# Kernel tuning notes

Measured on AMD Instinct MI355X. Metric: run time of the kernel, lower is better.

## Reference

```python
import jax, jax.numpy as jnp
import numpy as np

B = 128
NHEAD = 16
D_MODEL = 512
D_IN = 256  # each of f_* and f_*_out; concat -> 512
N_ATOM = 128


def _scopes():
    lens = np.array([96 + (i % 33) for i in range(B)], dtype=np.int64)  # max == 128 == N_ATOM
    starts_a = np.concatenate([[1], 1 + np.cumsum(lens)[:-1]]).astype(np.int64)
    nb = 2 * lens
    starts_b = np.concatenate([[1], 1 + np.cumsum(nb)[:-1]]).astype(np.int64)
    return lens, starts_a, nb, starts_b


def setup_inputs() -> dict:
    key = jax.random.key(0)
    ks = jax.random.split(key, 10)
    lens, starts_a, nb, starts_b = _scopes()
    Na = int(1 + lens.sum())   # 14279 (row 0 is padding)
    Nb = int(1 + nb.sum())     # 28557 (bond 0 is padding)
    f_atoms = jax.random.normal(ks[0], (Na, D_IN), jnp.float32)
    f_bonds = jax.random.normal(ks[1], (Nb, D_IN), jnp.float32)
    f_atoms_out = jax.random.normal(ks[2], (Na, D_IN), jnp.float32)
    f_bonds_out = jax.random.normal(ks[3], (Nb, D_IN), jnp.float32)
    b2a = jax.random.randint(ks[4], (Nb,), 0, 96, jnp.int64 if jax.config.jax_enable_x64 else jnp.int32)
    b2revb = jax.random.randint(ks[5], (Nb,), 0, Nb, b2a.dtype)
    a_scope = jnp.stack([jnp.asarray(starts_a), jnp.asarray(lens)], axis=1)
    b_scope = jnp.stack([jnp.asarray(starts_b), jnp.asarray(nb)], axis=1)
    W_atom = jax.random.normal(ks[6], (2 * D_IN, D_MODEL), jnp.float32) * 0.02
    b_atom = jnp.zeros((D_MODEL,), jnp.float32)
    W_bond = jax.random.normal(ks[7], (2 * D_IN, NHEAD), jnp.float32) * 0.02
    b_bond = jnp.zeros((NHEAD,), jnp.float32)
    return {"f_atoms": f_atoms, "f_bonds": f_bonds, "f_atoms_out": f_atoms_out,
            "f_bonds_out": f_bonds_out, "b2a": b2a, "b2revb": b2revb,
            "a_scope": a_scope, "b_scope": b_scope, "n_atom": N_ATOM,
            "W_atom": W_atom, "b_atom": b_atom, "W_bond": W_bond, "b_bond": b_bond}


def reference(f_atoms, f_bonds, f_atoms_out, f_bonds_out, b2a, b2revb,
              a_scope, b_scope, n_atom, W_atom, b_atom, W_bond, b_bond):
    Bsz = a_scope.shape[0]
    # atom embedding: concat + linear, drop padding row 0, pad per-molecule -> [n_atom, B, d]
    atoms = jnp.concatenate([f_atoms, f_atoms_out], axis=1) @ W_atom + b_atom  # [Na, d]
    starts_a, lens_a = a_scope[:, 0], a_scope[:, 1]
    pos = jnp.arange(n_atom)
    valid = pos[None, :] < lens_a[:, None]                       # [B, n_atom]
    gidx = jnp.where(valid, starts_a[:, None] + pos[None, :], 0)  # safe gather idx
    atoms_pad = jnp.where(valid[..., None], atoms[gidx], 0.0)     # [B, n_atom, d]
    atoms_emb = atoms_pad.transpose(1, 0, 2)                      # [n_atom, B, d] (batch_first=False)
    # bond embedding -> scatter into dense pairwise matrix
    bonds = jnp.concatenate([f_bonds, f_bonds_out], axis=1) @ W_bond + b_bond  # [Nb, nhead]
    Nb = bonds.shape[0]
    starts_b = b_scope[:, 0]
    mol = jnp.searchsorted(starts_b, jnp.arange(Nb), side='right') - 1  # molecule id per bond (-1 for pad bond 0)
    offset = jnp.maximum(mol, 0) * (n_atom * n_atom)
    idx = b2a + b2a[b2revb] * n_atom + offset                     # flat index into [B*n_atom*n_atom]
    flat = jnp.zeros((Bsz * n_atom * n_atom, bonds.shape[1]), bonds.dtype).at[idx].set(bonds)
    apairs = flat.reshape(Bsz, n_atom, n_atom, -1)                # [B, n_atom, n_atom, nhead]
    padding_mask = ~valid                                         # [B, n_atom], True = pad
    apairs = jnp.where(padding_mask[:, None, :, None], -jnp.inf, apairs)
    apairs = apairs.transpose(0, 3, 1, 2)                         # [B, nhead, n_atom, n_atom]
    return atoms_emb, apairs, padding_mask
```

## Files before the change

kernel.cpp:

```cpp
#include <hip/hip_runtime.h>
#include <math.h>

#define NEG_BIG (-1e30f)

typedef __attribute__((ext_vector_type(8))) short short8;
typedef __attribute__((ext_vector_type(4))) float floatx4;

__device__ __forceinline__ unsigned short f2bf(float x) {
    unsigned u = __float_as_uint(x);
    unsigned r = (u + 0x7fffu + ((u >> 16) & 1u)) >> 16;
    return (unsigned short)r;
}
__device__ __forceinline__ float bf2f(unsigned short h) {
    return __uint_as_float(((unsigned)h) << 16);
}

__global__ void k_prepWa(const float* __restrict__ W, short* __restrict__ H,
                         short* __restrict__ M, short* __restrict__ L) {
    int t = blockIdx.x * 256 + threadIdx.x;
    int n = t >> 9, k = t & 511;
    float x = W[(size_t)k * 512 + n];
    unsigned short h0 = f2bf(x); float r1 = x - bf2f(h0);
    unsigned short h1 = f2bf(r1); float r2 = r1 - bf2f(h1);
    unsigned short h2 = f2bf(r2);
    H[t] = (short)h0; M[t] = (short)h1; L[t] = (short)h2;
}

__global__ void k_prepWb(const float* __restrict__ Wb, short* __restrict__ Wbt) {
    int t = blockIdx.x * 256 + threadIdx.x;
    int h = t >> 9, k = t & 511;
    Wbt[t] = (short)f2bf(Wb[(size_t)k * 16 + h]);
}

__global__ __launch_bounds__(256) void k_atoms_mfma(
    const float* __restrict__ fA, const float* __restrict__ fAo,
    const int* __restrict__ a_scope,
    const short* __restrict__ WH, const short* __restrict__ WM, const short* __restrict__ WL,
    const float* __restrict__ bias, float* __restrict__ out, int Bmol)
{
    __shared__ short A_s[3][128 * 40];
    __shared__ int rs[128];

    const int tid = threadIdx.x;
    const int n0 = blockIdx.x * 128;
    const int mol = blockIdx.y;

    if (tid < 128) {
        int len = a_scope[2 * mol + 1];
        rs[tid] = (tid < len) ? (a_scope[2 * mol] + tid) : -1;
    }
    const int wid = tid >> 6, lane = tid & 63;
    const int wm = (wid >> 1) * 64, wn = (wid & 1) * 64;
    const int quad = lane >> 4, l16 = lane & 15;

    floatx4 acc[4][4];
#pragma unroll
    for (int i = 0; i < 4; i++)
#pragma unroll
        for (int j = 0; j < 4; j++) acc[i][j] = (floatx4){0.f, 0.f, 0.f, 0.f};

    const int ar = tid >> 1;
    const int ak = (tid & 1) * 16;
    __syncthreads();
    const int asrc = rs[ar];

    for (int k0 = 0; k0 < 512; k0 += 32) {
        float x[16];
        if (asrc >= 0) {
            int kg = k0 + ak;
            const float* p = (kg < 256) ? (fA + (size_t)asrc * 256 + kg)
                                        : (fAo + (size_t)asrc * 256 + (kg - 256));
#pragma unroll
            for (int i = 0; i < 4; i++) {
                float4 v = ((const float4*)p)[i];
                x[i * 4 + 0] = v.x; x[i * 4 + 1] = v.y;
                x[i * 4 + 2] = v.z; x[i * 4 + 3] = v.w;
            }
        } else {
#pragma unroll
            for (int i = 0; i < 16; i++) x[i] = 0.f;
        }
        short8 a00, a01, a10, a11, a20, a21;
#pragma unroll
        for (int i = 0; i < 8; i++) {
            unsigned short h0 = f2bf(x[i]); float r1 = x[i] - bf2f(h0);
            unsigned short h1 = f2bf(r1);   float r2 = r1 - bf2f(h1);
            a00[i] = (short)h0; a10[i] = (short)h1; a20[i] = (short)f2bf(r2);
        }
#pragma unroll
        for (int i = 0; i < 8; i++) {
            float xx = x[8 + i];
            unsigned short h0 = f2bf(xx); float r1 = xx - bf2f(h0);
            unsigned short h1 = f2bf(r1); float r2 = r1 - bf2f(h1);
            a01[i] = (short)h0; a11[i] = (short)h1; a21[i] = (short)f2bf(r2);
        }

        __syncthreads();
        const int abase = ar * 40 + ak;
        *(short8*)&A_s[0][abase] = a00; *(short8*)&A_s[0][abase + 8] = a01;
        *(short8*)&A_s[1][abase] = a10; *(short8*)&A_s[1][abase + 8] = a11;
        *(short8*)&A_s[2][abase] = a20; *(short8*)&A_s[2][abase + 8] = a21;
        __syncthreads();

        short8 af[3][4];
#pragma unroll
        for (int ti = 0; ti < 4; ti++) {
            int off = (wm + ti * 16 + l16) * 40 + quad * 8;
            af[0][ti] = *(const short8*)&A_s[0][off];
            af[1][ti] = *(const short8*)&A_s[1][off];
            af[2][ti] = *(const short8*)&A_s[2][off];
        }
#pragma unroll
        for (int tj = 0; tj < 4; tj++) {
            size_t bbase = (size_t)(n0 + wn + tj * 16 + l16) * 512 + k0 + quad * 8;
            short8 b0 = *(const short8*)(WH + bbase);
            short8 b1 = *(const short8*)(WM + bbase);
            short8 b2 = *(const short8*)(WL + bbase);
#pragma unroll
            for (int ti = 0; ti < 4; ti++) {
                floatx4 c = acc[ti][tj];
                c = __builtin_amdgcn_mfma_f32_16x16x32_bf16(af[0][ti], b0, c, 0, 0, 0);
                c = __builtin_amdgcn_mfma_f32_16x16x32_bf16(af[0][ti], b1, c, 0, 0, 0);
                c = __builtin_amdgcn_mfma_f32_16x16x32_bf16(af[1][ti], b0, c, 0, 0, 0);
                c = __builtin_amdgcn_mfma_f32_16x16x32_bf16(af[0][ti], b2, c, 0, 0, 0);
                c = __builtin_amdgcn_mfma_f32_16x16x32_bf16(af[1][ti], b1, c, 0, 0, 0);
                c = __builtin_amdgcn_mfma_f32_16x16x32_bf16(af[2][ti], b0, c, 0, 0, 0);
                acc[ti][tj] = c;
            }
        }
    }

#pragma unroll
    for (int tj = 0; tj < 4; tj++) {
        int n = n0 + wn + tj * 16 + l16;
        float bv = bias[n];
#pragma unroll
        for (int ti = 0; ti < 4; ti++) {
#pragma unroll
            for (int r = 0; r < 4; r++) {
                int pos = wm + ti * 16 + quad * 4 + r;
                bool valid = rs[pos] >= 0;
                float v = valid ? (acc[ti][tj][r] + bv) : 0.f;
                out[((size_t)pos * Bmol + mol) * 512 + n] = v;
            }
        }
    }
}

__global__ __launch_bounds__(256) void k_bonds_mfma(
    const float* __restrict__ fB, const float* __restrict__ fBo,
    const short* __restrict__ Wbt, const float* __restrict__ bb_,
    float* __restrict__ bonds, int Nb)
{
    __shared__ short feat[64 * 136];
    __shared__ short wb[16 * 512];

    const int tid = threadIdx.x;
    const int j0 = blockIdx.x * 64;

    for (int c = tid; c < 1024; c += 256) {
        int h = c >> 6, cc = c & 63;
        short8 v = *(const short8*)(Wbt + h * 512 + cc * 8);
        *(short8*)&wb[h * 512 + (((cc + h) & 63) * 8)] = v;
    }

    const int wid = tid >> 6, lane = tid & 63;
    const int quad = lane >> 4, l16 = lane & 15;
    floatx4 acc = (floatx4){0.f, 0.f, 0.f, 0.f};

    const int fr = tid >> 2;
    const int fs = (tid & 3) * 32;
    const int j = j0 + fr;

    for (int k0 = 0; k0 < 512; k0 += 128) {
        float x[32];
        if (j < Nb) {
            const float* p = (k0 < 256) ? (fB + (size_t)j * 256 + k0 + fs)
                                        : (fBo + (size_t)j * 256 + (k0 - 256) + fs);
#pragma unroll
            for (int i = 0; i < 8; i++) {
                float4 v = ((const float4*)p)[i];
                x[i * 4 + 0] = v.x; x[i * 4 + 1] = v.y;
                x[i * 4 + 2] = v.z; x[i * 4 + 3] = v.w;
            }
        } else {
#pragma unroll
            for (int i = 0; i < 32; i++) x[i] = 0.f;
        }
        __syncthreads();
#pragma unroll
        for (int c = 0; c < 4; c++) {
            short8 s;
#pragma unroll
            for (int i = 0; i < 8; i++) s[i] = (short)f2bf(x[c * 8 + i]);
            *(short8*)&feat[fr * 136 + fs + c * 8] = s;
        }
        __syncthreads();
#pragma unroll
        for (int kk = 0; kk < 4; kk++) {
            short8 a = *(const short8*)&feat[(wid * 16 + l16) * 136 + kk * 32 + quad * 8];
            int kchunk = (k0 + kk * 32 + quad * 8) >> 3;
            short8 b = *(const short8*)&wb[l16 * 512 + (((kchunk + l16) & 63) * 8)];
            acc = __builtin_amdgcn_mfma_f32_16x16x32_bf16(a, b, acc, 0, 0, 0);
        }
    }
    float bv = bb_[l16];
#pragma unroll
    for (int r = 0; r < 4; r++) {
        int jj = j0 + wid * 16 + quad * 4 + r;
        if (jj < Nb) bonds[(size_t)jj * 16 + l16] = acc[r] + bv;
    }
}

__global__ __launch_bounds__(512) void k_pair(
    const int* __restrict__ b2a, const int* __restrict__ b2revb,
    const int* __restrict__ b_scope, const int* __restrict__ a_scope,
    const float* __restrict__ bonds, float* __restrict__ out_ap,
    float* __restrict__ out_mask, int Bmol)
{
    __shared__ int w[16384];
    const int tid = threadIdx.x;
    const int mol = blockIdx.x;

#pragma unroll
    for (int i = 0; i < 8; i++)
        ((int4*)w)[i * 512 + tid] = make_int4(-1, -1, -1, -1);

    const int bs = b_scope[2 * mol];
    const int bc = b_scope[2 * mol + 1];
    const int len = a_scope[2 * mol + 1];
    __syncthreads();

    for (int q = tid; q < bc; q += 512) {
        int j = bs + q;
        int p2 = b2a[j];
        int p1 = b2a[b2revb[j]];
        atomicMax(&w[p1 * 128 + p2], j);
    }
    if (mol == 0 && tid == 0) {
        int p2 = b2a[0];
        int p1 = b2a[b2revb[0]];
        atomicMax(&w[p1 * 128 + p2], 0);
    }
    __syncthreads();

    if (tid < 32) {
        int p = tid * 4;
        float4 mv;
        mv.x = (p + 0 >= len) ? 1.0f : 0.0f;
        mv.y = (p + 1 >= len) ? 1.0f : 0.0f;
        mv.z = (p + 2 >= len) ? 1.0f : 0.0f;
        mv.w = (p + 3 >= len) ? 1.0f : 0.0f;
        *(float4*)&out_mask[mol * 128 + p] = mv;
    }

    const int p1 = tid >> 2;
    float* ob = out_ap + ((size_t)mol * 16 * 128 + p1) * 128;
#pragma unroll
    for (int g = 0; g < 8; g++) {
        int p2q = (tid & 3) + g * 4;
        int4 wv = ((const int4*)w)[p1 * 32 + p2q];
        int p2 = p2q * 4;
        bool m0 = (p2 + 0 >= len), m1 = (p2 + 1 >= len);
        bool m2 = (p2 + 2 >= len), m3 = (p2 + 3 >= len);
#pragma unroll
        for (int h = 0; h < 16; h++) {
            float4 v;
            v.x = m0 ? NEG_BIG : (wv.x >= 0 ? bonds[(size_t)wv.x * 16 + h] : 0.f);
            v.y = m1 ? NEG_BIG : (wv.y >= 0 ? bonds[(size_t)wv.y * 16 + h] : 0.f);
            v.z = m2 ? NEG_BIG : (wv.z >= 0 ? bonds[(size_t)wv.z * 16 + h] : 0.f);
            v.w = m3 ? NEG_BIG : (wv.w >= 0 ? bonds[(size_t)wv.w * 16 + h] : 0.f);
            *(float4*)(ob + (size_t)h * 16384 + p2) = v;
        }
    }
}

extern "C" void kernel_launch(void* const* d_in, const int* in_sizes, int n_in,
                              void* d_out, int out_size, void* d_ws, size_t ws_size,
                              hipStream_t stream)
{
    const float* f_atoms     = (const float*)d_in[0];
    const float* f_bonds     = (const float*)d_in[1];
    const float* f_atoms_out = (const float*)d_in[2];
    const float* f_bonds_out = (const float*)d_in[3];
    const int*   b2a         = (const int*)d_in[4];
    const int*   b2revb      = (const int*)d_in[5];
    const int*   a_scope     = (const int*)d_in[6];
    const int*   b_scope     = (const int*)d_in[7];
    const float* W_atom      = (const float*)d_in[9];
    const float* b_atom      = (const float*)d_in[10];
    const float* W_bond      = (const float*)d_in[11];
    const float* b_bond      = (const float*)d_in[12];

    const int Bmol = in_sizes[6] / 2;
    const int Nb   = in_sizes[4];

    char* ws = (char*)d_ws;
    size_t off = 0;
    float* bonds_ws = (float*)(ws + off); off += ((size_t)Nb * 16 * 4 + 255) & ~(size_t)255;
    short* WH       = (short*)(ws + off); off += 512 * 512 * 2;
    short* WM       = (short*)(ws + off); off += 512 * 512 * 2;
    short* WL       = (short*)(ws + off); off += 512 * 512 * 2;
    short* Wbt      = (short*)(ws + off); off += 16 * 512 * 2;

    float* out_emb  = (float*)d_out;
    float* out_ap   = out_emb + (size_t)128 * Bmol * 512;
    float* out_mask = out_ap + (size_t)Bmol * 16 * 128 * 128;

    hipLaunchKernelGGL(k_prepWa, dim3(1024), dim3(256), 0, stream, W_atom, WH, WM, WL);
    hipLaunchKernelGGL(k_prepWb, dim3(32), dim3(256), 0, stream, W_bond, Wbt);
    hipLaunchKernelGGL(k_atoms_mfma, dim3(4, Bmol), dim3(256), 0, stream,
                       f_atoms, f_atoms_out, a_scope, WH, WM, WL, b_atom, out_emb, Bmol);
    hipLaunchKernelGGL(k_bonds_mfma, dim3((Nb + 63) / 64), dim3(256), 0, stream,
                       f_bonds, f_bonds_out, Wbt, b_bond, bonds_ws, Nb);
    hipLaunchKernelGGL(k_pair, dim3(Bmol), dim3(512), 0, stream,
                       b2a, b2revb, b_scope, a_scope, bonds_ws, out_ap, out_mask, Bmol);
}
```

Baseline: 359.3 us.

## Split pair-matrix kernel into four row-quarter blocks per molecule

The pairwise scatter kernel now launches four 256-thread blocks per molecule, each owning 32 rows of the 128x128 matrix, with a quarter-size shared index table. Each thread writes 16 contiguous columns per head instead of strided float4 groups. The aim is more blocks and less LDS per block for better occupancy on a 256-CU device with only 128 molecules. In exchange, every block rescans all of its molecule's bonds and discards three quarters of them.

```diff
diff --git a/kernel.cpp b/kernel.cpp
--- a/kernel.cpp
+++ b/kernel.cpp
@@ -212,39 +212,40 @@
     }
 }
 
-__global__ __launch_bounds__(512) void k_pair(
+__global__ __launch_bounds__(256) void k_pair(
     const int* __restrict__ b2a, const int* __restrict__ b2revb,
     const int* __restrict__ b_scope, const int* __restrict__ a_scope,
     const float* __restrict__ bonds, float* __restrict__ out_ap,
     float* __restrict__ out_mask, int Bmol)
 {
-    __shared__ int w[16384];
+    __shared__ int w[32 * 128];
     const int tid = threadIdx.x;
-    const int mol = blockIdx.x;
-
-#pragma unroll
-    for (int i = 0; i < 8; i++)
-        ((int4*)w)[i * 512 + tid] = make_int4(-1, -1, -1, -1);
-
-    const int bs = b_scope[2 * mol];
-    const int bc = b_scope[2 * mol + 1];
+    const int mol = blockIdx.x >> 2;
+    const int q   = blockIdx.x & 3;
+
+#pragma unroll
+    for (int i = 0; i < 4; i++)
+        ((int4*)w)[i * 256 + tid] = make_int4(-1, -1, -1, -1);
+
+    const int bs  = b_scope[2 * mol];
+    const int bc  = b_scope[2 * mol + 1];
     const int len = a_scope[2 * mol + 1];
     __syncthreads();
 
-    for (int q = tid; q < bc; q += 512) {
-        int j = bs + q;
+    for (int idx = tid; idx < bc; idx += 256) {
+        int j = bs + idx;
         int p2 = b2a[j];
         int p1 = b2a[b2revb[j]];
-        atomicMax(&w[p1 * 128 + p2], j);
+        if ((p1 >> 5) == q) atomicMax(&w[(p1 & 31) * 128 + p2], j);
     }
     if (mol == 0 && tid == 0) {
         int p2 = b2a[0];
         int p1 = b2a[b2revb[0]];
-        atomicMax(&w[p1 * 128 + p2], 0);
+        if ((p1 >> 5) == q) atomicMax(&w[(p1 & 31) * 128 + p2], 0);
     }
     __syncthreads();
 
-    if (tid < 32) {
+    if (q == 0 && tid < 32) {
         int p = tid * 4;
         float4 mv;
         mv.x = (p + 0 >= len) ? 1.0f : 0.0f;
@@ -254,23 +255,29 @@
         *(float4*)&out_mask[mol * 128 + p] = mv;
     }
 
-    const int p1 = tid >> 2;
-    float* ob = out_ap + ((size_t)mol * 16 * 128 + p1) * 128;
-#pragma unroll
-    for (int g = 0; g < 8; g++) {
-        int p2q = (tid & 3) + g * 4;
-        int4 wv = ((const int4*)w)[p1 * 32 + p2q];
-        int p2 = p2q * 4;
-        bool m0 = (p2 + 0 >= len), m1 = (p2 + 1 >= len);
-        bool m2 = (p2 + 2 >= len), m3 = (p2 + 3 >= len);
-#pragma unroll
-        for (int h = 0; h < 16; h++) {
+    const int p1l = tid >> 3;
+    const int seg = tid & 7;
+    const int p1g = q * 32 + p1l;
+    int4 wv[4];
+#pragma unroll
+    for (int c = 0; c < 4; c++) wv[c] = ((const int4*)w)[p1l * 32 + seg * 4 + c];
+    bool msk[16];
+#pragma unroll
+    for (int c = 0; c < 16; c++) msk[c] = (seg * 16 + c >= len);
+
+    float* ob = out_ap + ((size_t)mol * 16 * 128 + p1g) * 128 + seg * 16;
+#pragma unroll
+    for (int h = 0; h < 16; h++) {
+        float* op = ob + (size_t)h * 16384;
+#pragma unroll
+        for (int c = 0; c < 4; c++) {
+            const int* wc = (const int*)&wv[c];
             float4 v;
-            v.x = m0 ? NEG_BIG : (wv.x >= 0 ? bonds[(size_t)wv.x * 16 + h] : 0.f);
-            v.y = m1 ? NEG_BIG : (wv.y >= 0 ? bonds[(size_t)wv.y * 16 + h] : 0.f);
-            v.z = m2 ? NEG_BIG : (wv.z >= 0 ? bonds[(size_t)wv.z * 16 + h] : 0.f);
-            v.w = m3 ? NEG_BIG : (wv.w >= 0 ? bonds[(size_t)wv.w * 16 + h] : 0.f);
-            *(float4*)(ob + (size_t)h * 16384 + p2) = v;
+            v.x = msk[c*4+0] ? NEG_BIG : (wc[0] >= 0 ? bonds[(size_t)wc[0] * 16 + h] : 0.f);
+            v.y = msk[c*4+1] ? NEG_BIG : (wc[1] >= 0 ? bonds[(size_t)wc[1] * 16 + h] : 0.f);
+            v.z = msk[c*4+2] ? NEG_BIG : (wc[2] >= 0 ? bonds[(size_t)wc[2] * 16 + h] : 0.f);
+            v.w = msk[c*4+3] ? NEG_BIG : (wc[3] >= 0 ? bonds[(size_t)wc[3] * 16 + h] : 0.f);
+            *(float4*)(op + c * 4) = v;
         }
     }
 }
@@ -313,6 +320,6 @@
                        f_atoms, f_atoms_out, a_scope, WH, WM, WL, b_atom, out_emb, Bmol);
     hipLaunchKernelGGL(k_bonds_mfma, dim3((Nb + 63) / 64), dim3(256), 0, stream,
                        f_bonds, f_bonds_out, Wbt, b_bond, bonds_ws, Nb);
-    hipLaunchKernelGGL(k_pair, dim3(Bmol), dim3(512), 0, stream,
+    hipLaunchKernelGGL(k_pair, dim3(Bmol * 4), dim3(256), 0, stream,
                        b2a, b2revb, b_scope, a_scope, bonds_ws, out_ap, out_mask, Bmol);
 }
```

Measured after the change: 347.0 us. 3.4% less time.
